# Optimization experiments

Hardware: AMD Instinct MI355X
Metric: run time of the kernel (lower is better)

Reference implementation:

```python
import jax, jax.numpy as jnp
import numpy as np

DIM = 192
HEADS = 6
HIDDEN = 384  # int(dim * mlp_ratio)


def conv2d(x, w, b=None, padding=0, groups=1):
    out = jax.lax.conv_general_dilated(
        x, w, (1, 1), [(padding, padding), (padding, padding)],
        feature_group_count=groups,
        dimension_numbers=('NCHW', 'OIHW', 'NCHW'))
    return out if b is None else out + b[None, :, None, None]


def layernorm(x, g, b, eps=1e-5):
    m = x.mean(-1, keepdims=True)
    v = x.var(-1, keepdims=True)  # biased, matches torch LayerNorm
    return (x - m) / jnp.sqrt(v + eps) * g + b


def l2norm(x, eps=1e-12):  # F.normalize(dim=-1)
    n = jnp.linalg.norm(x, axis=-1, keepdims=True)
    return x / jnp.maximum(n, eps)


def setup_inputs() -> dict:
    key = jax.random.key(0)
    ks = jax.random.split(key, 12)
    s = 0.02
    return {
        'x': jax.random.normal(ks[0], (4, DIM, 128, 128), dtype=jnp.float32),
        'g1': jnp.ones((DIM,), jnp.float32),
        'b1': jnp.zeros((DIM,), jnp.float32),
        'w_qkv': jax.random.normal(ks[1], (3 * DIM, DIM, 1, 1), jnp.float32) * s,
        'w_dw': jax.random.normal(ks[2], (3 * DIM, 1, 3, 3), jnp.float32) * s,
        'temp': jnp.ones((HEADS, 1, 1), jnp.float32),
        'w_head': jax.random.normal(ks[3], (HEADS, HEADS, 3, 3), jnp.float32) * s,
        'w_proj': jax.random.normal(ks[4], (DIM, DIM, 1, 1), jnp.float32) * s,
        'g2': jnp.ones((DIM,), jnp.float32),
        'b2': jnp.zeros((DIM,), jnp.float32),
        'w_fc1': jax.random.normal(ks[5], (HIDDEN, DIM), jnp.float32) * s,
        'b_fc1': jnp.zeros((HIDDEN,), jnp.float32),
        'w_fc2': jax.random.normal(ks[6], (DIM, HIDDEN), jnp.float32) * s,
        'b_fc2': jnp.zeros((DIM,), jnp.float32),
        'w_sa': jax.random.normal(ks[7], (1, DIM, 3, 3), jnp.float32) * s,
        'b_sa': jnp.zeros((1,), jnp.float32),
    }


def reference(x, g1, b1, w_qkv, w_dw, temp, w_head, w_proj, g2, b2,
              w_fc1, b_fc1, w_fc2, b_fc2, w_sa, b_sa):
    b, c, h, w = x.shape
    hw = h * w
    # norm1 (note: original code re-assigns x, so residual uses normed x)
    xf = x.reshape(b, c, hw).transpose(0, 2, 1)          # [b, hw, c]
    x1 = layernorm(xf, g1, b1).transpose(0, 2, 1).reshape(b, c, h, w)
    # channel attention (Restormer style)
    qkv = conv2d(conv2d(x1, w_qkv), w_dw, padding=1, groups=3 * c)
    q, k, v = jnp.split(qkv, 3, axis=1)
    cp = c // HEADS
    q = l2norm(q.reshape(b, HEADS, cp, hw))
    k = l2norm(k.reshape(b, HEADS, cp, hw))
    v = v.reshape(b, HEADS, cp, hw)
    attn = jnp.einsum('bhcn,bhdn->bhcd', q, k) * temp    # [b, heads, cp, cp]
    attn = conv2d(attn, w_head, padding=1)               # conv over head channels
    attn = jax.nn.softmax(attn, axis=-1)
    out = jnp.einsum('bhcd,bhdn->bhcn', attn, v).reshape(b, c, h, w)
    out = conv2d(out, w_proj)
    x2 = x1 + out
    # MLP branch with spatial-gating attn
    x3 = x2.reshape(b, c, hw).transpose(0, 2, 1)         # [b, hw, c]
    y = layernorm(x3, g2, b2)
    y = jax.nn.gelu(y @ w_fc1.T + b_fc1, approximate=False)
    y = y @ w_fc2.T + b_fc2
    y = jax.nn.gelu(y, approximate=False)                # SAAttn act_fn
    y4 = y.reshape(b, h, w, c).transpose(0, 3, 1, 2)     # [b, c, h, w]
    gate = jax.nn.sigmoid(conv2d(y4, w_sa, b_sa, padding=1))  # [b,1,h,w]
    y = (y4 * gate).reshape(b, c, hw).transpose(0, 2, 1)
    x4 = x3 + y
    return x4.transpose(0, 2, 1).reshape(b, c, h, w)
```

## Files before the change

### kernel.cpp

```cpp
#include <hip/hip_runtime.h>
#include <hip/hip_bf16.h>
#include <math.h>

using bf16 = __hip_bfloat16;

static constexpr int CDIM   = 192;
static constexpr int HEADS  = 6;
static constexpr int CP     = 32;
static constexpr int HIDDEN = 384;
static constexpr int HImg   = 128;
static constexpr int WImg   = 128;
static constexpr int HW     = HImg * WImg;
static constexpr int BATCH  = 4;
static constexpr int PCHUNK = 256;
static constexpr int CSPLIT = 12;

typedef __attribute__((ext_vector_type(8))) short short8;
typedef __attribute__((ext_vector_type(4))) float f32x4;
typedef __attribute__((ext_vector_type(4))) unsigned short ushort4v;
typedef __attribute__((ext_vector_type(8))) unsigned short ushort8v;

template<typename T> __device__ inline float tof(T v);
template<> __device__ inline float tof<float>(float v){ return v; }
template<> __device__ inline float tof<bf16>(bf16 v){ return __bfloat162float(v); }

template<typename T> __device__ inline T fromf(float v);
template<> __device__ inline float fromf<float>(float v){ return v; }
template<> __device__ inline bf16  fromf<bf16>(float v){ return __float2bfloat16(v); }

__device__ inline unsigned short f2bf_bits(float f){
    bf16 h = __float2bfloat16(f);
    return *reinterpret_cast<unsigned short*>(&h);
}
__device__ inline float bfbits2f(unsigned short u){
    union { unsigned int i; float f; } c; c.i = ((unsigned int)u) << 16; return c.f;
}

__device__ inline float gelu_exact(float x){
    return 0.5f * x * (1.0f + erff(x * 0.70710678118654752440f));
}

__device__ inline void load4f(const float* p, float* f){
    f32x4 v = *reinterpret_cast<const f32x4*>(p);
    f[0]=v[0]; f[1]=v[1]; f[2]=v[2]; f[3]=v[3];
}
__device__ inline void load4f(const bf16* p, float* f){
    ushort4v v = *reinterpret_cast<const ushort4v*>(p);
    f[0]=bfbits2f(v[0]); f[1]=bfbits2f(v[1]); f[2]=bfbits2f(v[2]); f[3]=bfbits2f(v[3]);
}

__device__ __forceinline__ void gload16(const bf16* g, bf16* l){
    __builtin_amdgcn_global_load_lds(
        (const __attribute__((address_space(1))) void*)g,
        (__attribute__((address_space(3))) void*)l, 16, 0, 0);
}

__global__ __launch_bounds__(256) void convw_kernel(
    const float* __restrict__ w_qkv, const float* __restrict__ w_proj,
    const float* __restrict__ w_fc1, const float* __restrict__ w_fc2,
    bf16* __restrict__ wq, bf16* __restrict__ wp,
    bf16* __restrict__ wf1, bf16* __restrict__ wf2)
{
    int i = blockIdx.x * 256 + threadIdx.x;
    const int n0 = 576*192, n1 = n0 + 192*192, n2 = n1 + 384*192, n3 = n2 + 192*384;
    if (i < n0)      wq[i]       = fromf<bf16>(w_qkv[i]);
    else if (i < n1) wp[i - n0]  = fromf<bf16>(w_proj[i - n0]);
    else if (i < n2) wf1[i - n1] = fromf<bf16>(w_fc1[i - n1]);
    else if (i < n3) wf2[i - n2] = fromf<bf16>(w_fc2[i - n2]);
}

template<typename T, bool WRES>
__global__ __launch_bounds__(256) void ln_fused_kernel(
    const T* __restrict__ in, const float* __restrict__ g,
    const float* __restrict__ b, bf16* __restrict__ resF, bf16* __restrict__ outT)
{
    int z = blockIdx.y, p0 = blockIdx.x * 64;
    __shared__ float tile[CDIM][65];
    __shared__ float sred[4][64], s2red[4][64];
    __shared__ float mrow[64], rrow[64];
    const T* ib = in + (size_t)z * CDIM * HW + p0;
    int tid = threadIdx.x;
    for (int j = tid; j < CDIM * 16; j += 256){
        int c = j >> 4, p4 = (j & 15) * 4;
        float f[4];
        load4f(ib + (size_t)c * HW + p4, f);
        tile[c][p4]   = f[0]; tile[c][p4+1] = f[1];
        tile[c][p4+2] = f[2]; tile[c][p4+3] = f[3];
    }
    __syncthreads();
    int p = tid & 63, q = tid >> 6;
    float s = 0.f, s2 = 0.f;
    #pragma unroll 4
    for (int c = q * 48; c < q * 48 + 48; ++c){
        float v = tile[c][p]; s += v; s2 += v * v;
    }
    sred[q][p] = s; s2red[q][p] = s2;
    __syncthreads();
    if (tid < 64){
        float ts = sred[0][tid] + sred[1][tid] + sred[2][tid] + sred[3][tid];
        float t2 = s2red[0][tid] + s2red[1][tid] + s2red[2][tid] + s2red[3][tid];
        float mean = ts * (1.0f / CDIM);
        float var  = t2 * (1.0f / CDIM) - mean * mean;
        mrow[tid] = mean;
        rrow[tid] = rsqrtf(var + 1e-5f);
    }
    __syncthreads();
    unsigned short* oT = (unsigned short*)(outT + ((size_t)z * HW + p0) * CDIM);
    for (int j = tid; j < 64 * 48; j += 256){
        int pr = j / 48, c4 = (j % 48) * 4;
        float m = mrow[pr], r = rrow[pr];
        ushort4v o;
        #pragma unroll
        for (int k = 0; k < 4; ++k){
            int c = c4 + k;
            o[k] = f2bf_bits((tile[c][pr] - m) * r * g[c] + b[c]);
        }
        *(ushort4v*)&oT[(size_t)pr * CDIM + c4] = o;
    }
    if (WRES){
        unsigned short* oF = (unsigned short*)resF + (size_t)z * CDIM * HW + p0;
        for (int j = tid; j < CDIM * 16; j += 256){
            int c = j >> 4, p4 = (j & 15) * 4;
            float gg = g[c], bb = b[c];
            ushort4v v;
            #pragma unroll
            for (int k = 0; k < 4; ++k)
                v[k] = f2bf_bits((tile[c][p4 + k] - mrow[p4 + k]) * rrow[p4 + k] * gg + bb);
            *(ushort4v*)&oF[(size_t)c * HW + p4] = v;
        }
    }
}

template<int EPI>
__global__ __launch_bounds__(256) void gemm_mfma_kernel(
    const bf16* __restrict__ Wb, const bf16* __restrict__ XT,
    void* __restrict__ Cout, const float* __restrict__ bias,
    const bf16* __restrict__ res, int M, int K)
{
    __shared__ bf16 smem[12288];
    bf16* Als = smem;
    bf16* Bls = smem + 4096;
    int z  = blockIdx.z;
    int n0 = blockIdx.x * 128;
    int m0 = blockIdx.y * 64;
    const bf16* Xb = XT + (size_t)z * HW * K;
    int tid  = threadIdx.x;
    int lane = tid & 63, wid = tid >> 6;
    int wm = wid & 1, wn = wid >> 1;
    int r16 = lane & 15, grp = lane >> 4;

    f32x4 acc[2][4];
    #pragma unroll
    for (int i = 0; i < 2; ++i)
        #pragma unroll
        for (int j = 0; j < 4; ++j){ f32x4 zz = {0.f,0.f,0.f,0.f}; acc[i][j] = zz; }

    int nkt = K >> 6;
    for (int kt = 0; kt < nkt; ++kt){
        #pragma unroll
        for (int i = 0; i < 2; ++i){
            int s = i * 256 + tid;
            int row = s >> 3, ch = s & 7;
            const bf16* g = Wb + (size_t)(m0 + row) * K + kt * 64 + ((ch ^ (row & 7)) * 8);
            gload16(g, Als + s * 8);
        }
        #pragma unroll
        for (int i = 0; i < 4; ++i){
            int s = i * 256 + tid;
            int row = s >> 3, ch = s & 7;
            const bf16* g = Xb + (size_t)(n0 + row) * K + kt * 64 + ((ch ^ (row & 7)) * 8);
            gload16(g, Bls + s * 8);
        }
        asm volatile("s_waitcnt vmcnt(0)" ::: "memory");
        __syncthreads();
        #pragma unroll
        for (int ks = 0; ks < 2; ++ks){
            int kel = ks * 32 + grp * 8;
            short8 a[2], b[4];
            #pragma unroll
            for (int fi = 0; fi < 2; ++fi){
                int row = wm * 32 + fi * 16 + r16;
                a[fi] = *reinterpret_cast<const short8*>(Als + row * 64 + (kel ^ ((row & 7) * 8)));
            }
            #pragma unroll
            for (int fj = 0; fj < 4; ++fj){
                int row = wn * 64 + fj * 16 + r16;
                b[fj] = *reinterpret_cast<const short8*>(Bls + row * 64 + (kel ^ ((row & 7) * 8)));
            }
            #pragma unroll
            for (int fi = 0; fi < 2; ++fi)
                #pragma unroll
                for (int fj = 0; fj < 4; ++fj)
                    acc[fi][fj] = __builtin_amdgcn_mfma_f32_16x16x32_bf16(
                        a[fi], b[fj], acc[fi][fj], 0, 0, 0);
        }
        __syncthreads();
    }

    if (EPI == 3){
        unsigned short* T = (unsigned short*)smem;
        #pragma unroll
        for (int fi = 0; fi < 2; ++fi)
            #pragma unroll
            for (int fj = 0; fj < 4; ++fj){
                int nl = wn * 64 + fj * 16 + r16;
                int mb = wm * 32 + fi * 16 + grp * 4;
                #pragma unroll
                for (int rr = 0; rr < 4; ++rr){
                    float v = gelu_exact(acc[fi][fj][rr] + bias[m0 + mb + rr]);
                    T[nl * 72 + mb + rr] = f2bf_bits(v);
                }
            }
        __syncthreads();
        bf16* Y = (bf16*)Cout;
        int rrow = tid >> 1, half = tid & 1;
        const short8* srcv = reinterpret_cast<const short8*>(T + rrow * 72 + half * 32);
        short8* dstv = reinterpret_cast<short8*>(
            Y + ((size_t)z * HW + n0 + rrow) * M + m0 + half * 32);
        #pragma unroll
        for (int i = 0; i < 4; ++i) dstv[i] = srcv[i];
        return;
    }

    bf16* Cb = (bf16*)Cout;
    #pragma unroll
    for (int fi = 0; fi < 2; ++fi)
        #pragma unroll
        for (int fj = 0; fj < 4; ++fj){
            int mb = m0 + wm * 32 + fi * 16 + grp * 4;
            int n  = n0 + wn * 64 + fj * 16 + r16;
            #pragma unroll
            for (int rr = 0; rr < 4; ++rr){
                float v = acc[fi][fj][rr];
                int m = mb + rr;
                if (EPI == 1) v += tof<bf16>(res[(size_t)z * M * HW + (size_t)m * HW + n]);
                if (EPI == 2) v = gelu_exact(v + bias[m]);
                Cb[(size_t)z * M * HW + (size_t)m * HW + n] = fromf<bf16>(v);
            }
        }
}

__global__ __launch_bounds__(256) void dw_kernel(
    const bf16* __restrict__ in, const float* __restrict__ wdw,
    bf16* __restrict__ out, float* __restrict__ sqp)
{
    int ch = blockIdx.y, z = blockIdx.z;
    int tid = threadIdx.x;
    int idx = blockIdx.x * 2048 + tid * 8;
    int yy = idx >> 7, xx = idx & 127;
    const unsigned short* p =
        (const unsigned short*)(in + ((size_t)z * 3 * CDIM + ch) * HW);
    float w[9];
    #pragma unroll
    for (int t = 0; t < 9; ++t) w[t] = wdw[ch * 9 + t];
    float f[3][8], lf[3], rf[3];
    #pragma unroll
    for (int dy = 0; dy < 3; ++dy){
        int iy = yy + dy - 1;
        if (iy >= 0 && iy < HImg){
            ushort8v v8 = *(const ushort8v*)(p + iy * WImg + xx);
            #pragma unroll
            for (int j = 0; j < 8; ++j) f[dy][j] = bfbits2f(v8[j]);
        } else {
            #pragma unroll
            for (int j = 0; j < 8; ++j) f[dy][j] = 0.f;
        }
        float l = __shfl_up(f[dy][7], 1);
        float r = __shfl_down(f[dy][0], 1);
        lf[dy] = (xx == 0) ? 0.f : l;
        rf[dy] = (xx + 8 >= WImg) ? 0.f : r;
    }
    ushort8v o8;
    float sq = 0.f;
    #pragma unroll
    for (int j = 0; j < 8; ++j){
        float a = 0.f;
        #pragma unroll
        for (int dy = 0; dy < 3; ++dy){
            float e0 = (j == 0) ? lf[dy] : f[dy][j - 1];
            float e2 = (j == 7) ? rf[dy] : f[dy][j + 1];
            a = fmaf(w[dy*3], e0, fmaf(w[dy*3+1], f[dy][j], fmaf(w[dy*3+2], e2, a)));
        }
        o8[j] = f2bf_bits(a);
        sq = fmaf(a, a, sq);
    }
    *(ushort8v*)((unsigned short*)(out + ((size_t)z * 3 * CDIM + ch) * HW) + idx) = o8;
    if (ch < 2 * CDIM){
        #pragma unroll
        for (int m = 1; m < 64; m <<= 1) sq += __shfl_xor(sq, m, 64);
        __shared__ float red[4];
        if ((tid & 63) == 0) red[tid >> 6] = sq;
        __syncthreads();
        if (tid == 0)
            sqp[((size_t)ch * BATCH + z) * 8 + blockIdx.x] =
                red[0] + red[1] + red[2] + red[3];
    }
}

__global__ __launch_bounds__(256) void attn_qk_kernel(
    const bf16* __restrict__ qkv, const float* __restrict__ sqp,
    const float* __restrict__ temp, float* __restrict__ part)
{
    int chunk = blockIdx.x;
    int h = blockIdx.y, z = blockIdx.z;
    __shared__ unsigned short qs[CP][PCHUNK + 4];
    __shared__ unsigned short ks[CP][PCHUNK + 4];
    __shared__ float invqs[CP], invks[CP];
    int tid = threadIdx.x;
    if (tid < 2 * CP){
        int which = tid >> 5, cc = tid & 31;
        int ch = which * CDIM + h * CP + cc;
        const float* sp = &sqp[((size_t)ch * BATCH + z) * 8];
        float s = sp[0]+sp[1]+sp[2]+sp[3]+sp[4]+sp[5]+sp[6]+sp[7];
        float inv = 1.0f / fmaxf(sqrtf(s), 1e-12f);
        (which ? invks : invqs)[cc] = inv;
    }
    int n0 = chunk * PCHUNK;
    const unsigned short* qb = (const unsigned short*)(qkv + ((size_t)z * 3 * CDIM + h * CP) * HW);
    const unsigned short* kb = (const unsigned short*)(qkv + ((size_t)z * 3 * CDIM + CDIM + h * CP) * HW);
    for (int i = tid; i < CP * (PCHUNK / 4); i += 256){
        int r = i >> 6, p4 = i & 63;
        *(ushort4v*)&qs[r][p4 * 4] = *(const ushort4v*)&qb[(size_t)r * HW + n0 + p4 * 4];
        *(ushort4v*)&ks[r][p4 * 4] = *(const ushort4v*)&kb[(size_t)r * HW + n0 + p4 * 4];
    }
    __syncthreads();
    int c  = tid >> 3;
    int d0 = (tid & 7) * 4;
    float acc[4] = {0.f, 0.f, 0.f, 0.f};
    for (int p4 = 0; p4 < PCHUNK / 4; ++p4){
        ushort4v qv = *(const ushort4v*)&qs[c][p4 * 4];
        float qf0 = bfbits2f(qv[0]), qf1 = bfbits2f(qv[1]);
        float qf2 = bfbits2f(qv[2]), qf3 = bfbits2f(qv[3]);
        #pragma unroll
        for (int j = 0; j < 4; ++j){
            ushort4v kv = *(const ushort4v*)&ks[d0 + j][p4 * 4];
            acc[j] = fmaf(qf0, bfbits2f(kv[0]),
                     fmaf(qf1, bfbits2f(kv[1]),
                     fmaf(qf2, bfbits2f(kv[2]),
                     fmaf(qf3, bfbits2f(kv[3]), acc[j]))));
        }
    }
    float sc = invqs[c] * temp[h];
    size_t base = ((size_t)chunk * BATCH * HEADS + (size_t)z * HEADS + h) * CP * CP
                + c * CP + d0;
    #pragma unroll
    for (int j = 0; j < 4; ++j)
        part[base + j] = acc[j] * sc * invks[d0 + j];
}

__global__ __launch_bounds__(256) void attn_reduce_kernel(
    const float* __restrict__ part, float* __restrict__ attn)
{
    int idx = blockIdx.x * 256 + threadIdx.x;
    float s = 0.f;
    for (int ch = 0; ch < HW / PCHUNK; ++ch)
        s += part[(size_t)ch * (BATCH * HEADS * CP * CP) + idx];
    attn[idx] = s;
}

__global__ __launch_bounds__(256) void headconv_softmax_kernel(
    const float* __restrict__ attn, const float* __restrict__ wh,
    float* __restrict__ attn2)
{
    int oh = blockIdx.x, z = blockIdx.y;
    __shared__ float wsm[HEADS * 9];
    __shared__ float ain[HEADS][CP * CP];
    __shared__ float aout[CP * CP];
    int tid = threadIdx.x;
    if (tid < HEADS * 9) wsm[tid] = wh[oh * HEADS * 9 + tid];
    for (int i = tid; i < HEADS * CP * CP; i += 256)
        ain[i >> 10][i & 1023] = attn[((size_t)z * HEADS + (i >> 10)) * CP * CP + (i & 1023)];
    __syncthreads();
    for (int idx = tid; idx < CP * CP; idx += 256){
        int i = idx >> 5, j = idx & 31;
        float acc = 0.f;
        #pragma unroll
        for (int ih = 0; ih < HEADS; ++ih){
            #pragma unroll
            for (int dy = 0; dy < 3; ++dy){
                int ii = i + dy - 1;
                if (ii < 0 || ii >= CP) continue;
                #pragma unroll
                for (int dx = 0; dx < 3; ++dx){
                    int jj = j + dx - 1;
                    if (jj < 0 || jj >= CP) continue;
                    acc += wsm[ih * 9 + dy * 3 + dx] * ain[ih][ii * CP + jj];
                }
            }
        }
        aout[idx] = acc;
    }
    __syncthreads();
    int r = tid >> 3, l8 = tid & 7;
    float v[4];
    #pragma unroll
    for (int k = 0; k < 4; ++k) v[k] = aout[r * CP + l8 * 4 + k];
    float mx = fmaxf(fmaxf(v[0], v[1]), fmaxf(v[2], v[3]));
    #pragma unroll
    for (int m = 1; m < 8; m <<= 1) mx = fmaxf(mx, __shfl_xor(mx, m, 64));
    float sum = 0.f;
    #pragma unroll
    for (int k = 0; k < 4; ++k){ v[k] = expf(v[k] - mx); sum += v[k]; }
    #pragma unroll
    for (int m = 1; m < 8; m <<= 1) sum += __shfl_xor(sum, m, 64);
    float rs = 1.0f / sum;
    float* o = attn2 + ((size_t)z * HEADS + oh) * CP * CP + r * CP + l8 * 4;
    #pragma unroll
    for (int k = 0; k < 4; ++k) o[k] = v[k] * rs;
}

__global__ __launch_bounds__(256) void av_kernel(
    const float* __restrict__ attn2, const bf16* __restrict__ qkv, bf16* __restrict__ outT)
{
    int h = blockIdx.y, z = blockIdx.z;
    int tid = threadIdx.x;
    __shared__ float As[CP][CP];
    __shared__ unsigned short Vs[CP][PCHUNK];
    __shared__ unsigned short ot[256][36];
    for (int i = tid; i < CP * CP; i += 256)
        As[i >> 5][i & 31] = attn2[((size_t)(z * HEADS + h)) * CP * CP + i];
    int n0 = blockIdx.x * 256;
    const unsigned short* vb =
        (const unsigned short*)(qkv + ((size_t)z * 3 * CDIM + 2 * CDIM + h * CP) * HW) + n0;
    for (int i = tid; i < CP * 64; i += 256){
        int d = i >> 6, p4 = (i & 63) * 4;
        *(ushort4v*)&Vs[d][p4] = *(const ushort4v*)(vb + (size_t)d * HW + p4);
    }
    __syncthreads();
    float vreg[CP];
    #pragma unroll
    for (int d = 0; d < CP; ++d) vreg[d] = bfbits2f(Vs[d][tid]);
    for (int c = 0; c < CP; ++c){
        float acc = 0.f;
        #pragma unroll
        for (int d = 0; d < CP; ++d) acc = fmaf(As[c][d], vreg[d], acc);
        ot[tid][c] = f2bf_bits(acc);
    }
    __syncthreads();
    unsigned short* ob = (unsigned short*)outT
        + ((size_t)z * HW + (size_t)n0) * CDIM + h * CP;
    for (int j = tid; j < 256 * 8; j += 256){
        int row = j >> 3, q4 = (j & 7) * 4;
        *(ushort4v*)&ob[(size_t)row * CDIM + q4] = *(ushort4v*)&ot[row][q4];
    }
}

__global__ __launch_bounds__(256) void gate_partial_kernel(
    const bf16* __restrict__ y, const float* __restrict__ wsa,
    float* __restrict__ part_g)
{
    int cs = blockIdx.y, z = blockIdx.z;
    __shared__ float wsm[16 * 9];
    if (threadIdx.x < 144) wsm[threadIdx.x] = wsa[cs * 144 + threadIdx.x];
    __syncthreads();
    int idx = blockIdx.x * 2048 + threadIdx.x * 8;
    int yy = idx >> 7, xx = idx & 127;
    const unsigned short* yb =
        (const unsigned short*)(y + (size_t)z * CDIM * HW + (size_t)cs * 16 * HW);
    float acc[8] = {0.f,0.f,0.f,0.f,0.f,0.f,0.f,0.f};
    for (int c = 0; c < 16; ++c){
        const unsigned short* pc = yb + (size_t)c * HW;
        #pragma unroll
        for (int dy = 0; dy < 3; ++dy){
            int iy = yy + dy - 1;
            float f[8], lf, rf;
            if (iy >= 0 && iy < HImg){
                ushort8v v8 = *(const ushort8v*)(pc + iy * WImg + xx);
                #pragma unroll
                for (int j = 0; j < 8; ++j) f[j] = bfbits2f(v8[j]);
            } else {
                #pragma unroll
                for (int j = 0; j < 8; ++j) f[j] = 0.f;
            }
            float l = __shfl_up(f[7], 1);
            float r = __shfl_down(f[0], 1);
            lf = (xx == 0) ? 0.f : l;
            rf = (xx + 8 >= WImg) ? 0.f : r;
            const float* wr = &wsm[c * 9 + dy * 3];
            #pragma unroll
            for (int j = 0; j < 8; ++j){
                float e0 = (j == 0) ? lf : f[j - 1];
                float e2 = (j == 7) ? rf : f[j + 1];
                acc[j] = fmaf(wr[0], e0, fmaf(wr[1], f[j], fmaf(wr[2], e2, acc[j])));
            }
        }
    }
    float* og = &part_g[((size_t)cs * BATCH + z) * HW + idx];
    f32x4 o0 = {acc[0], acc[1], acc[2], acc[3]};
    f32x4 o1 = {acc[4], acc[5], acc[6], acc[7]};
    *(f32x4*)og = o0;
    *(f32x4*)(og + 4) = o1;
}

__global__ __launch_bounds__(256) void gate_finish_kernel(
    const float* __restrict__ part_g, const float* __restrict__ bsa,
    float* __restrict__ gate)
{
    int i4 = (blockIdx.x * 256 + threadIdx.x) * 4;
    float b0 = bsa[0];
    f32x4 acc = {b0, b0, b0, b0};
    #pragma unroll
    for (int cs = 0; cs < CSPLIT; ++cs){
        f32x4 v = *(const f32x4*)&part_g[(size_t)cs * BATCH * HW + i4];
        #pragma unroll
        for (int j = 0; j < 4; ++j) acc[j] += v[j];
    }
    f32x4 o;
    #pragma unroll
    for (int j = 0; j < 4; ++j) o[j] = 1.0f / (1.0f + expf(-acc[j]));
    *(f32x4*)&gate[i4] = o;
}

__global__ __launch_bounds__(256) void final_kernel(
    const bf16* __restrict__ x2, const bf16* __restrict__ y2,
    const float* __restrict__ gate, float* __restrict__ out)
{
    size_t i8 = ((size_t)blockIdx.x * 256 + threadIdx.x) * 8;
    int n = (int)(i8 % HW);
    int z = (int)(i8 / ((size_t)CDIM * HW));
    ushort8v a8 = *(const ushort8v*)((const unsigned short*)x2 + i8);
    ushort8v b8 = *(const ushort8v*)((const unsigned short*)y2 + i8);
    const float* gp = gate + (size_t)z * HW + n;
    f32x4 g0 = *(const f32x4*)gp;
    f32x4 g1 = *(const f32x4*)(gp + 4);
    f32x4 o0, o1;
    #pragma unroll
    for (int j = 0; j < 4; ++j){
        o0[j] = bfbits2f(a8[j])     + bfbits2f(b8[j])     * g0[j];
        o1[j] = bfbits2f(a8[j + 4]) + bfbits2f(b8[j + 4]) * g1[j];
    }
    *(f32x4*)(out + i8) = o0;
    *(f32x4*)(out + i8 + 4) = o1;
}

extern "C" void kernel_launch(void* const* d_in, const int* in_sizes, int n_in,
                              void* d_out, int out_size, void* d_ws, size_t ws_size,
                              hipStream_t stream)
{
    const float* x      = (const float*)d_in[0];
    const float* g1     = (const float*)d_in[1];
    const float* b1     = (const float*)d_in[2];
    const float* w_qkv  = (const float*)d_in[3];
    const float* w_dw   = (const float*)d_in[4];
    const float* temp   = (const float*)d_in[5];
    const float* w_head = (const float*)d_in[6];
    const float* w_proj = (const float*)d_in[7];
    const float* g2     = (const float*)d_in[8];
    const float* b2     = (const float*)d_in[9];
    const float* w_fc1  = (const float*)d_in[10];
    const float* b_fc1  = (const float*)d_in[11];
    const float* w_fc2  = (const float*)d_in[12];
    const float* b_fc2  = (const float*)d_in[13];
    const float* w_sa   = (const float*)d_in[14];
    const float* b_sa   = (const float*)d_in[15];
    float* out = (float*)d_out;

    char* ws = (char*)d_ws;
    const size_t FULL = (size_t)BATCH * CDIM * HW;

    bf16* x1 = (bf16*)ws;
    bf16* y2 = x1;
    char* R1 = ws + FULL * 2;
    bf16*  qkvA      = (bf16*)R1;
    bf16*  attn_outT = (bf16*)R1;
    bf16*  ln2T      = (bf16*)R1;
    bf16*  y1T       = (bf16*)(R1 + FULL * 2);
    char* R2 = R1 + FULL * 3 * 2;
    bf16*  x1T = (bf16*)R2;
    bf16*  dwB = (bf16*)R2;
    bf16*  x2  = (bf16*)R2;
    char* SM = R2 + FULL * 3 * 2;
    float* attn   = (float*)SM;
    float* attn2  = attn + BATCH * HEADS * CP * CP;
    float* gate   = attn2 + BATCH * HEADS * CP * CP;
    float* sqp    = gate + BATCH * HW;
    float* part   = sqp + 2 * CDIM * BATCH * 8;
    float* part_g = part;
    bf16* wq_b  = (bf16*)(part + (HW / PCHUNK) * BATCH * HEADS * CP * CP);
    bf16* wp_b  = wq_b  + 576 * 192;
    bf16* wf1_b = wp_b  + 192 * 192;
    bf16* wf2_b = wf1_b + 384 * 192;

    dim3 blk(256);

    convw_kernel<<<dim3((294912 + 255) / 256), blk, 0, stream>>>(
        w_qkv, w_proj, w_fc1, w_fc2, wq_b, wp_b, wf1_b, wf2_b);
    ln_fused_kernel<float, true><<<dim3(HW / 64, BATCH), blk, 0, stream>>>(
        x, g1, b1, x1, x1T);
    gemm_mfma_kernel<0><<<dim3(HW / 128, (3 * CDIM) / 64, BATCH), blk, 0, stream>>>(
        wq_b, x1T, qkvA, nullptr, nullptr, 3 * CDIM, CDIM);
    dw_kernel<<<dim3(HW / 2048, 3 * CDIM, BATCH), blk, 0, stream>>>(qkvA, w_dw, dwB, sqp);
    attn_qk_kernel<<<dim3(HW / PCHUNK, HEADS, BATCH), blk, 0, stream>>>(
        dwB, sqp, temp, part);
    attn_reduce_kernel<<<dim3((BATCH * HEADS * CP * CP) / 256), blk, 0, stream>>>(part, attn);
    headconv_softmax_kernel<<<dim3(HEADS, BATCH), blk, 0, stream>>>(attn, w_head, attn2);
    av_kernel<<<dim3(HW / 256, HEADS, BATCH), blk, 0, stream>>>(attn2, dwB, attn_outT);
    gemm_mfma_kernel<1><<<dim3(HW / 128, CDIM / 64, BATCH), blk, 0, stream>>>(
        wp_b, attn_outT, x2, nullptr, x1, CDIM, CDIM);
    ln_fused_kernel<bf16, false><<<dim3(HW / 64, BATCH), blk, 0, stream>>>(
        x2, g2, b2, nullptr, ln2T);
    gemm_mfma_kernel<3><<<dim3(HW / 128, HIDDEN / 64, BATCH), blk, 0, stream>>>(
        wf1_b, ln2T, y1T, b_fc1, nullptr, HIDDEN, CDIM);
    gemm_mfma_kernel<2><<<dim3(HW / 128, CDIM / 64, BATCH), blk, 0, stream>>>(
        wf2_b, y1T, y2, b_fc2, nullptr, CDIM, HIDDEN);
    gate_partial_kernel<<<dim3(HW / 2048, CSPLIT, BATCH), blk, 0, stream>>>(
        y2, w_sa, part_g);
    gate_finish_kernel<<<dim3(BATCH * HW / 1024), blk, 0, stream>>>(part_g, b_sa, gate);
    final_kernel<<<dim3((int)(FULL / 2048)), blk, 0, stream>>>(x2, y2, gate, out);
}
```

Baseline: 287.4 us.

## Double-buffer GEMM tiles, widen N tile to 256, and stage epilogue through LDS

The MFMA GEMM now prefetches the next K tile into a second LDS buffer while computing the current one, waiting on a partial vmcnt instead of draining all loads. The N tile grows from 128 to 256, with each wave covering all 64 M rows, so A fragments are reused across more columns. Non-transposed epilogues now go through LDS so each thread writes 16-byte vectors, with bias, GELU and residual applied on bf16-rounded values. LDS use rises to 80KB per block, which lowers occupancy and halves the grid size.

```diff
diff --git a/kernel.cpp b/kernel.cpp
--- a/kernel.cpp
+++ b/kernel.cpp
@@ -137,107 +137,143 @@
     void* __restrict__ Cout, const float* __restrict__ bias,
     const bf16* __restrict__ res, int M, int K)
 {
-    __shared__ bf16 smem[12288];
-    bf16* Als = smem;
-    bf16* Bls = smem + 4096;
+    __shared__ bf16 smem[40960];
+    bf16* Ab0 = smem;
+    bf16* Ab1 = smem + 4096;
+    bf16* Bb0 = smem + 8192;
+    bf16* Bb1 = smem + 8192 + 16384;
     int z  = blockIdx.z;
-    int n0 = blockIdx.x * 128;
+    int n0 = blockIdx.x * 256;
     int m0 = blockIdx.y * 64;
-    const bf16* Xb = XT + (size_t)z * HW * K;
+    const bf16* Xb = XT + (size_t)z * (size_t)HW * K;
     int tid  = threadIdx.x;
     int lane = tid & 63, wid = tid >> 6;
-    int wm = wid & 1, wn = wid >> 1;
     int r16 = lane & 15, grp = lane >> 4;
 
-    f32x4 acc[2][4];
-    #pragma unroll
-    for (int i = 0; i < 2; ++i)
+    f32x4 acc[4][4];
+    #pragma unroll
+    for (int i = 0; i < 4; ++i)
         #pragma unroll
         for (int j = 0; j < 4; ++j){ f32x4 zz = {0.f,0.f,0.f,0.f}; acc[i][j] = zz; }
 
-    int nkt = K >> 6;
-    for (int kt = 0; kt < nkt; ++kt){
+    auto STAGE = [&](int kt, int buf){
+        bf16* Al = buf ? Ab1 : Ab0;
+        bf16* Bl = buf ? Bb1 : Bb0;
         #pragma unroll
         for (int i = 0; i < 2; ++i){
             int s = i * 256 + tid;
             int row = s >> 3, ch = s & 7;
-            const bf16* g = Wb + (size_t)(m0 + row) * K + kt * 64 + ((ch ^ (row & 7)) * 8);
-            gload16(g, Als + s * 8);
-        }
-        #pragma unroll
-        for (int i = 0; i < 4; ++i){
+            gload16(Wb + (size_t)(m0 + row) * K + kt * 64 + ((ch ^ (row & 7)) * 8),
+                    Al + s * 8);
+        }
+        #pragma unroll
+        for (int i = 0; i < 8; ++i){
             int s = i * 256 + tid;
             int row = s >> 3, ch = s & 7;
-            const bf16* g = Xb + (size_t)(n0 + row) * K + kt * 64 + ((ch ^ (row & 7)) * 8);
-            gload16(g, Bls + s * 8);
-        }
-        asm volatile("s_waitcnt vmcnt(0)" ::: "memory");
-        __syncthreads();
+            gload16(Xb + (size_t)(n0 + row) * K + kt * 64 + ((ch ^ (row & 7)) * 8),
+                    Bl + s * 8);
+        }
+    };
+
+    int nkt = K >> 6;
+    STAGE(0, 0);
+    int cur = 0;
+    for (int kt = 0; kt < nkt; ++kt){
+        if (kt + 1 < nkt){
+            STAGE(kt + 1, cur ^ 1);
+            asm volatile("s_waitcnt vmcnt(10)" ::: "memory");
+        } else {
+            asm volatile("s_waitcnt vmcnt(0)" ::: "memory");
+        }
+        __builtin_amdgcn_s_barrier();
+        bf16* Al = cur ? Ab1 : Ab0;
+        bf16* Bl = cur ? Bb1 : Bb0;
         #pragma unroll
         for (int ks = 0; ks < 2; ++ks){
             int kel = ks * 32 + grp * 8;
-            short8 a[2], b[4];
-            #pragma unroll
-            for (int fi = 0; fi < 2; ++fi){
-                int row = wm * 32 + fi * 16 + r16;
-                a[fi] = *reinterpret_cast<const short8*>(Als + row * 64 + (kel ^ ((row & 7) * 8)));
+            short8 a[4], b[4];
+            #pragma unroll
+            for (int f = 0; f < 4; ++f){
+                int arow = f * 16 + r16;
+                a[f] = *reinterpret_cast<const short8*>(Al + arow * 64 + (kel ^ ((arow & 7) * 8)));
+                int brow = wid * 64 + f * 16 + r16;
+                b[f] = *reinterpret_cast<const short8*>(Bl + brow * 64 + (kel ^ ((brow & 7) * 8)));
             }
             #pragma unroll
-            for (int fj = 0; fj < 4; ++fj){
-                int row = wn * 64 + fj * 16 + r16;
-                b[fj] = *reinterpret_cast<const short8*>(Bls + row * 64 + (kel ^ ((row & 7) * 8)));
-            }
-            #pragma unroll
-            for (int fi = 0; fi < 2; ++fi)
+            for (int fi = 0; fi < 4; ++fi)
                 #pragma unroll
                 for (int fj = 0; fj < 4; ++fj)
                     acc[fi][fj] = __builtin_amdgcn_mfma_f32_16x16x32_bf16(
                         a[fi], b[fj], acc[fi][fj], 0, 0, 0);
         }
-        __syncthreads();
+        asm volatile("s_waitcnt lgkmcnt(0)" ::: "memory");
+        __builtin_amdgcn_s_barrier();
+        cur ^= 1;
     }
 
     if (EPI == 3){
         unsigned short* T = (unsigned short*)smem;
         #pragma unroll
-        for (int fi = 0; fi < 2; ++fi)
+        for (int fi = 0; fi < 4; ++fi)
             #pragma unroll
             for (int fj = 0; fj < 4; ++fj){
-                int nl = wn * 64 + fj * 16 + r16;
-                int mb = wm * 32 + fi * 16 + grp * 4;
+                int nl = wid * 64 + fj * 16 + r16;
+                int mb = fi * 16 + grp * 4;
                 #pragma unroll
                 for (int rr = 0; rr < 4; ++rr){
                     float v = gelu_exact(acc[fi][fj][rr] + bias[m0 + mb + rr]);
                     T[nl * 72 + mb + rr] = f2bf_bits(v);
                 }
             }
-        __syncthreads();
+        asm volatile("s_waitcnt lgkmcnt(0)" ::: "memory");
+        __builtin_amdgcn_s_barrier();
         bf16* Y = (bf16*)Cout;
-        int rrow = tid >> 1, half = tid & 1;
-        const short8* srcv = reinterpret_cast<const short8*>(T + rrow * 72 + half * 32);
+        const short8* srcv = reinterpret_cast<const short8*>(T + tid * 72);
         short8* dstv = reinterpret_cast<short8*>(
-            Y + ((size_t)z * HW + n0 + rrow) * M + m0 + half * 32);
-        #pragma unroll
-        for (int i = 0; i < 4; ++i) dstv[i] = srcv[i];
+            Y + ((size_t)z * HW + n0 + tid) * M + m0);
+        #pragma unroll
+        for (int i = 0; i < 8; ++i) dstv[i] = srcv[i];
         return;
     }
 
-    bf16* Cb = (bf16*)Cout;
-    #pragma unroll
-    for (int fi = 0; fi < 2; ++fi)
-        #pragma unroll
-        for (int fj = 0; fj < 4; ++fj){
-            int mb = m0 + wm * 32 + fi * 16 + grp * 4;
-            int n  = n0 + wn * 64 + fj * 16 + r16;
-            #pragma unroll
-            for (int rr = 0; rr < 4; ++rr){
-                float v = acc[fi][fj][rr];
-                int m = mb + rr;
-                if (EPI == 1) v += tof<bf16>(res[(size_t)z * M * HW + (size_t)m * HW + n]);
-                if (EPI == 2) v = gelu_exact(v + bias[m]);
-                Cb[(size_t)z * M * HW + (size_t)m * HW + n] = fromf<bf16>(v);
+    {
+        unsigned short* T = (unsigned short*)smem;
+        #pragma unroll
+        for (int fi = 0; fi < 4; ++fi)
+            #pragma unroll
+            for (int fj = 0; fj < 4; ++fj){
+                int m = fi * 16 + grp * 4;
+                int n = wid * 64 + fj * 16 + r16;
+                #pragma unroll
+                for (int rr = 0; rr < 4; ++rr)
+                    T[(m + rr) * 264 + n] = f2bf_bits(acc[fi][fj][rr]);
             }
-        }
+        asm volatile("s_waitcnt lgkmcnt(0)" ::: "memory");
+        __builtin_amdgcn_s_barrier();
+        int row = tid >> 2, c8 = (tid & 3) * 8;
+        bf16* Cb = (bf16*)Cout;
+        size_t gbase = (size_t)z * M * HW + (size_t)(m0 + row) * HW + n0 + c8;
+        float bv = (EPI == 2) ? bias[m0 + row] : 0.f;
+        #pragma unroll
+        for (int j = 0; j < 8; ++j){
+            int coff = j * 32;
+            ushort8v t8 = *(const ushort8v*)&T[row * 264 + c8 + coff];
+            ushort8v o8;
+            if (EPI == 0){
+                o8 = t8;
+            } else if (EPI == 1){
+                ushort8v r8 = *(const ushort8v*)((const unsigned short*)res + gbase + coff);
+                #pragma unroll
+                for (int k = 0; k < 8; ++k)
+                    o8[k] = f2bf_bits(bfbits2f(t8[k]) + bfbits2f(r8[k]));
+            } else {
+                #pragma unroll
+                for (int k = 0; k < 8; ++k)
+                    o8[k] = f2bf_bits(gelu_exact(bfbits2f(t8[k]) + bv));
+            }
+            *(ushort8v*)((unsigned short*)Cb + gbase + coff) = o8;
+        }
+    }
 }
 
 __global__ __launch_bounds__(256) void dw_kernel(
@@ -587,7 +623,7 @@
         w_qkv, w_proj, w_fc1, w_fc2, wq_b, wp_b, wf1_b, wf2_b);
     ln_fused_kernel<float, true><<<dim3(HW / 64, BATCH), blk, 0, stream>>>(
         x, g1, b1, x1, x1T);
-    gemm_mfma_kernel<0><<<dim3(HW / 128, (3 * CDIM) / 64, BATCH), blk, 0, stream>>>(
+    gemm_mfma_kernel<0><<<dim3(HW / 256, (3 * CDIM) / 64, BATCH), blk, 0, stream>>>(
         wq_b, x1T, qkvA, nullptr, nullptr, 3 * CDIM, CDIM);
     dw_kernel<<<dim3(HW / 2048, 3 * CDIM, BATCH), blk, 0, stream>>>(qkvA, w_dw, dwB, sqp);
     attn_qk_kernel<<<dim3(HW / PCHUNK, HEADS, BATCH), blk, 0, stream>>>(
@@ -595,13 +631,13 @@
     attn_reduce_kernel<<<dim3((BATCH * HEADS * CP * CP) / 256), blk, 0, stream>>>(part, attn);
     headconv_softmax_kernel<<<dim3(HEADS, BATCH), blk, 0, stream>>>(attn, w_head, attn2);
     av_kernel<<<dim3(HW / 256, HEADS, BATCH), blk, 0, stream>>>(attn2, dwB, attn_outT);
-    gemm_mfma_kernel<1><<<dim3(HW / 128, CDIM / 64, BATCH), blk, 0, stream>>>(
+    gemm_mfma_kernel<1><<<dim3(HW / 256, CDIM / 64, BATCH), blk, 0, stream>>>(
         wp_b, attn_outT, x2, nullptr, x1, CDIM, CDIM);
     ln_fused_kernel<bf16, false><<<dim3(HW / 64, BATCH), blk, 0, stream>>>(
         x2, g2, b2, nullptr, ln2T);
-    gemm_mfma_kernel<3><<<dim3(HW / 128, HIDDEN / 64, BATCH), blk, 0, stream>>>(
+    gemm_mfma_kernel<3><<<dim3(HW / 256, HIDDEN / 64, BATCH), blk, 0, stream>>>(
         wf1_b, ln2T, y1T, b_fc1, nullptr, HIDDEN, CDIM);
-    gemm_mfma_kernel<2><<<dim3(HW / 128, CDIM / 64, BATCH), blk, 0, stream>>>(
+    gemm_mfma_kernel<2><<<dim3(HW / 256, CDIM / 64, BATCH), blk, 0, stream>>>(
         wf2_b, y1T, y2, b_fc2, nullptr, CDIM, HIDDEN);
     gate_partial_kernel<<<dim3(HW / 2048, CSPLIT, BATCH), blk, 0, stream>>>(
         y2, w_sa, part_g);
```

After: 315.3 us. +9.7%, slower.
